# Kernel optimization log

Hardware: AMD Instinct MI355X
Metric: run time of the kernel (lower is better)

The kernel has to match this reference:

```python
import jax, jax.numpy as jnp
import numpy as np


def _grid_sample_3d(vol, grid):
    """Trilinear 3D grid_sample, zero padding, align_corners=False (torch default).

    vol:  [B, C, D, H, W]
    grid: [B, P, 3] normalized coords in [-1, 1]; grid[...,0]->W axis,
          grid[...,1]->H axis, grid[...,2]->D axis (torch convention).
    returns [B, C, P]
    """
    B, C, D, H, W = vol.shape
    x = (grid[..., 0] + 1.0) * (W * 0.5) - 0.5
    y = (grid[..., 1] + 1.0) * (H * 0.5) - 0.5
    z = (grid[..., 2] + 1.0) * (D * 0.5) - 0.5
    x0, y0, z0 = jnp.floor(x), jnp.floor(y), jnp.floor(z)
    gather = jax.vmap(lambda v, zz, yy, xx: v[:, zz, yy, xx])  # per-batch gather -> [C, P]
    out = jnp.zeros((B, C, x.shape[1]), vol.dtype)
    for dz in (0.0, 1.0):
        for dy in (0.0, 1.0):
            for dx in (0.0, 1.0):
                xi, yi, zi = x0 + dx, y0 + dy, z0 + dz
                w = (1.0 - jnp.abs(x - xi)) * (1.0 - jnp.abs(y - yi)) * (1.0 - jnp.abs(z - zi))
                valid = (xi >= 0) & (xi < W) & (yi >= 0) & (yi < H) & (zi >= 0) & (zi < D)
                xc = jnp.clip(xi, 0, W - 1).astype(jnp.int32)
                yc = jnp.clip(yi, 0, H - 1).astype(jnp.int32)
                zc = jnp.clip(zi, 0, D - 1).astype(jnp.int32)
                vals = gather(vol, zc, yc, xc)  # [B, C, P]
                out = out + vals * jnp.where(valid, w, 0.0)[:, None, :]
    return out


def _offset_grid(xs, A, Wk):
    """xs: [N,3] sample points; A: [N,3,3]; Wk: [3,K] offset weights.
    Returns [N, K, 3] grid coords ordered (z_feat, y_feat, x_feat) as in the torch code."""
    off = jnp.einsum('nij,jk->nik', A, Wk)  # bmm with repeated weight -> [N,3,K]
    xf = xs[:, 2:3] + off[:, 0, :]
    yf = xs[:, 1:2] + off[:, 1, :]
    zf = xs[:, 0:1] + off[:, 2, :]
    return jnp.stack([zf, yf, xf], axis=-1)


def setup_inputs() -> dict:
    key = jax.random.key(0)
    k1, k2, k3, k4 = jax.random.split(key, 4)
    B, C, D, H, W = 2, 16, 96, 96, 96
    Feats, K = 512, 1024
    inp = jax.random.normal(k1, (B, C, D, H, W), jnp.float32)
    xyz_sample = jax.random.uniform(k2, (B, Feats, 3), jnp.float32, -1.0, 1.0)
    A = jax.random.normal(k3, (B * Feats, 3, 3), jnp.float32) * 0.1
    weight = jax.random.normal(k4, (6, K), jnp.float32) * 0.05  # xyz_off.weight
    return {"input": inp, "xyz_sample": xyz_sample, "A": A, "weight": weight}


def reference(input, xyz_sample, A, weight):
    B, Feats, _ = xyz_sample.shape
    C = input.shape[1]
    K = weight.shape[1]  # 1024
    xs = xyz_sample.reshape(B * Feats, 3)
    g1 = _offset_grid(xs, A, weight[:3]).reshape(B, Feats * K, 3)
    g2 = _offset_grid(xs, A, weight[3:]).reshape(B, Feats * K, 3)
    feats = _grid_sample_3d(input, g1) - _grid_sample_3d(input, g2)  # [B, C, Feats*K]
    return feats.reshape(B, C * Feats, K)
```

## Files before the change

### kernel.cpp

```cpp
#include <hip/hip_runtime.h>


#define NB 2
#define NC 16
#define NS 96
#define NS3 (NS * NS * NS)
#define FEATS 512
#define NK 1024
#define KSPLIT 2
#define KCHUNK (NK / KSPLIT)
#define PASSES 4

#define RVOX 8
#define VSTRIDE 48

__device__ __forceinline__ unsigned int bfround(float f) {
  unsigned int u = __float_as_uint(f);
  return (u + 0x7fffu + ((u >> 16) & 1u)) >> 16;
}

#define BLO(v) __uint_as_float((v) << 16)
#define BHI(v) __uint_as_float((v) & 0xffff0000u)

__device__ __forceinline__ void tri_duo(
    const float* __restrict__ vol, size_t cbase,
    const unsigned char* __restrict__ sp,
    int ox0, int oy0, int oz0,
    float x, float y, float z, float sgn, float acc[8]) {
  float fx0 = floorf(x), fy0 = floorf(y), fz0 = floorf(z);
  int ix0 = (int)fx0, iy0 = (int)fy0, iz0 = (int)fz0;
  float tx = x - fx0, ty = y - fy0, tz = z - fz0;
  float wxa[2] = {1.0f - tx, tx};
  float wya[2] = {1.0f - ty, ty};
  float wza[2] = {1.0f - tz, tz};

  int lx0 = ix0 - ox0, ly0 = iy0 - oy0, lz0 = iz0 - oz0;
  bool fast = ((unsigned)lx0 < 7u) & ((unsigned)ly0 < 7u) & ((unsigned)lz0 < 7u);

  if (__builtin_expect(fast, 1)) {
#pragma unroll
    for (int dz = 0; dz < 2; dz++) {
      float wz = sgn * wza[dz];
#pragma unroll
      for (int dy = 0; dy < 2; dy++) {
        float wzy = wz * wya[dy];
        const unsigned char* rp =
            sp + (((lz0 + dz) * RVOX + (ly0 + dy)) * RVOX + lx0) * VSTRIDE;
#pragma unroll
        for (int dx = 0; dx < 2; dx++) {
          float w = wzy * wxa[dx];
          uint4 u = *(const uint4*)(rp + dx * VSTRIDE);
          acc[0] += w * BLO(u.x);
          acc[1] += w * BHI(u.x);
          acc[2] += w * BLO(u.y);
          acc[3] += w * BHI(u.y);
          acc[4] += w * BLO(u.z);
          acc[5] += w * BHI(u.z);
          acc[6] += w * BLO(u.w);
          acc[7] += w * BHI(u.w);
        }
      }
    }
  } else {
#pragma unroll
    for (int dz = 0; dz < 2; dz++) {
      int zc = iz0 + dz;
      if ((unsigned)zc >= (unsigned)NS) continue;
#pragma unroll
      for (int dy = 0; dy < 2; dy++) {
        int yc = iy0 + dy;
        if ((unsigned)yc >= (unsigned)NS) continue;
        float wzy = sgn * wza[dz] * wya[dy];
#pragma unroll
        for (int dx = 0; dx < 2; dx++) {
          int xc = ix0 + dx;
          if ((unsigned)xc >= (unsigned)NS) continue;
          float w = wzy * wxa[dx];
          const float* p = vol + cbase + (((size_t)zc * NS + yc) * NS + xc);
#pragma unroll
          for (int c = 0; c < 8; c++)
            acc[c] += w * p[(size_t)c * NS3];
        }
      }
    }
  }
}

__global__ __launch_bounds__(256) void sample_fused(
    const float* __restrict__ vol, const float* __restrict__ xyz,
    const float* __restrict__ A, const float* __restrict__ weight,
    float* __restrict__ out) {
  __shared__ __align__(16) unsigned char stage[RVOX * RVOX * RVOX * VSTRIDE];

  int bid = blockIdx.x;
  int kseg = bid & (KSPLIT - 1);
  int n = bid >> 1;
  int b = n >> 9;
  int f = n & 511;
  int kbase = kseg * KCHUNK;
  int tid = threadIdx.x;

  const float* Xn = xyz + (size_t)n * 3;
  float bx = (Xn[0] + 1.0f) * 48.0f - 0.5f;
  float by = (Xn[1] + 1.0f) * 48.0f - 0.5f;
  float bz = (Xn[2] + 1.0f) * 48.0f - 0.5f;
  int ox0 = (int)floorf(bx) - 3;
  int oy0 = (int)floorf(by) - 3;
  int oz0 = (int)floorf(bz) - 3;

  int duo = tid & 1;
  int ksub = tid >> 1;

  float wreg[PASSES][6];
#pragma unroll
  for (int p = 0; p < PASSES; p++) {
    int k = kbase + p * 128 + ksub;
#pragma unroll
    for (int q = 0; q < 6; q++) wreg[p][q] = weight[q * NK + k];
  }

  const float* An = A + (size_t)n * 9;
  float a00 = An[0], a01 = An[1], a02 = An[2];
  float a10 = An[3], a11 = An[4], a12 = An[5];
  float a20 = An[6], a21 = An[7], a22 = An[8];

  size_t vb = (size_t)b * NC * NS3;
#pragma unroll
  for (int j = 0; j < 4; j++) {
    int w = tid + 256 * j;
    int half = w & 1;
    int v = w >> 1;
    int xg = v & 7, yg = (v >> 3) & 7, zg = v >> 6;
    int xc = ox0 + xg, yc = oy0 + yg, zc = oz0 + zg;
    uint4 r = make_uint4(0u, 0u, 0u, 0u);
    if (((unsigned)xc < (unsigned)NS) & ((unsigned)yc < (unsigned)NS) &
        ((unsigned)zc < (unsigned)NS)) {
      const float* p = vol + vb + (size_t)(half * 8) * NS3 +
                       (((size_t)zc * NS + yc) * NS + xc);
      float f0 = p[0];
      float f1 = p[NS3];
      float f2 = p[2 * NS3];
      float f3 = p[3 * NS3];
      float f4 = p[4 * NS3];
      float f5 = p[5 * NS3];
      float f6 = p[6 * NS3];
      float f7 = p[7 * NS3];
      r.x = bfround(f0) | (bfround(f1) << 16);
      r.y = bfround(f2) | (bfround(f3) << 16);
      r.z = bfround(f4) | (bfround(f5) << 16);
      r.w = bfround(f6) | (bfround(f7) << 16);
    }
    *(uint4*)(stage + (size_t)v * VSTRIDE + half * 16) = r;
  }
  __syncthreads();

  const unsigned char* sp = stage + duo * 16;
  size_t cbase = ((size_t)b * NC + duo * 8) * NS3;
  size_t obase = (size_t)b * (NC * FEATS * NK) +
                 (size_t)(duo * 8) * (FEATS * NK) + (size_t)f * NK + kbase;

#pragma unroll
  for (int pass = 0; pass < PASSES; pass++) {
    int kl = pass * 128 + ksub;
    float w0 = wreg[pass][0];
    float w1 = wreg[pass][1];
    float w2 = wreg[pass][2];
    float w3 = wreg[pass][3];
    float w4 = wreg[pass][4];
    float w5 = wreg[pass][5];

    float acc[8] = {0.0f, 0.0f, 0.0f, 0.0f, 0.0f, 0.0f, 0.0f, 0.0f};

    {
      float oz = a00 * w0 + a01 * w1 + a02 * w2;
      float oy = a10 * w0 + a11 * w1 + a12 * w2;
      float ox = a20 * w0 + a21 * w1 + a22 * w2;
      tri_duo(vol, cbase, sp, ox0, oy0, oz0, bx + ox * 48.0f, by + oy * 48.0f,
              bz + oz * 48.0f, 1.0f, acc);
    }
    {
      float oz = a00 * w3 + a01 * w4 + a02 * w5;
      float oy = a10 * w3 + a11 * w4 + a12 * w5;
      float ox = a20 * w3 + a21 * w4 + a22 * w5;
      tri_duo(vol, cbase, sp, ox0, oy0, oz0, bx + ox * 48.0f, by + oy * 48.0f,
              bz + oz * 48.0f, -1.0f, acc);
    }

    size_t o = obase + kl;
#pragma unroll
    for (int c = 0; c < 8; c++)
      out[o + (size_t)c * (FEATS * NK)] = acc[c];
  }
}

extern "C" void kernel_launch(void* const* d_in, const int* in_sizes, int n_in,
                              void* d_out, int out_size, void* d_ws,
                              size_t ws_size, hipStream_t stream) {
  const float* vol    = (const float*)d_in[0];
  const float* xyz    = (const float*)d_in[1];
  const float* A      = (const float*)d_in[2];
  const float* weight = (const float*)d_in[3];
  float* out = (float*)d_out;

  sample_fused<<<NB * FEATS * KSPLIT, 256, 0, stream>>>(vol, xyz, A, weight,
                                                        out);
}
```

Baseline: 200.0 us.

## Drop K-split, swizzle LDS staging layout, and software-pipeline weight loads

Each block now handles all 1024 offsets for one feature point, so the 8x8x8 neighbourhood is staged into shared memory once instead of twice. The stage moves to a 64-byte stride with an XOR swizzle on the y/x and z/half bits to cut LDS bank conflicts on the uint4 reads. Weight loads are prefetched one pass ahead in a rolled loop instead of all preloaded into registers. The trade-off is half as many blocks (less parallelism and tail balance), larger shared memory per block, and more address arithmetic per sample.

```diff
diff --git a/kernel.cpp b/kernel.cpp
--- a/kernel.cpp
+++ b/kernel.cpp
@@ -7,12 +7,16 @@
 #define NS3 (NS * NS * NS)
 #define FEATS 512
 #define NK 1024
-#define KSPLIT 2
-#define KCHUNK (NK / KSPLIT)
-#define PASSES 4
+#define PASSES 8
 
 #define RVOX 8
-#define VSTRIDE 48
+
+__device__ __forceinline__ int stage_addr(int xg, int yg, int zg, int h) {
+  int v = (zg << 6) + (yg << 3) + xg;
+  int sw1 = (yg ^ (xg >> 1)) & 1;
+  int sw2 = (h ^ zg) & 1;
+  return (v << 6) | (sw1 << 5) | (sw2 << 4);
+}
 
 __device__ __forceinline__ unsigned int bfround(float f) {
   unsigned int u = __float_as_uint(f);
@@ -24,7 +28,7 @@
 
 __device__ __forceinline__ void tri_duo(
     const float* __restrict__ vol, size_t cbase,
-    const unsigned char* __restrict__ sp,
+    const unsigned char* __restrict__ stage, int duo,
     int ox0, int oy0, int oz0,
     float x, float y, float z, float sgn, float acc[8]) {
   float fx0 = floorf(x), fy0 = floorf(y), fz0 = floorf(z);
@@ -41,15 +45,16 @@
 #pragma unroll
     for (int dz = 0; dz < 2; dz++) {
       float wz = sgn * wza[dz];
+      int vz = lz0 + dz;
 #pragma unroll
       for (int dy = 0; dy < 2; dy++) {
         float wzy = wz * wya[dy];
-        const unsigned char* rp =
-            sp + (((lz0 + dz) * RVOX + (ly0 + dy)) * RVOX + lx0) * VSTRIDE;
+        int vy = ly0 + dy;
 #pragma unroll
         for (int dx = 0; dx < 2; dx++) {
           float w = wzy * wxa[dx];
-          uint4 u = *(const uint4*)(rp + dx * VSTRIDE);
+          int vx = lx0 + dx;
+          uint4 u = *(const uint4*)(stage + stage_addr(vx, vy, vz, duo));
           acc[0] += w * BLO(u.x);
           acc[1] += w * BHI(u.x);
           acc[2] += w * BLO(u.y);
@@ -90,14 +95,11 @@
     const float* __restrict__ vol, const float* __restrict__ xyz,
     const float* __restrict__ A, const float* __restrict__ weight,
     float* __restrict__ out) {
-  __shared__ __align__(16) unsigned char stage[RVOX * RVOX * RVOX * VSTRIDE];
-
-  int bid = blockIdx.x;
-  int kseg = bid & (KSPLIT - 1);
-  int n = bid >> 1;
+  __shared__ __align__(128) unsigned char stage[RVOX * RVOX * RVOX * 64];
+
+  int n = blockIdx.x;
   int b = n >> 9;
   int f = n & 511;
-  int kbase = kseg * KCHUNK;
   int tid = threadIdx.x;
 
   const float* Xn = xyz + (size_t)n * 3;
@@ -110,14 +112,6 @@
 
   int duo = tid & 1;
   int ksub = tid >> 1;
-
-  float wreg[PASSES][6];
-#pragma unroll
-  for (int p = 0; p < PASSES; p++) {
-    int k = kbase + p * 128 + ksub;
-#pragma unroll
-    for (int q = 0; q < 6; q++) wreg[p][q] = weight[q * NK + k];
-  }
 
   const float* An = A + (size_t)n * 9;
   float a00 = An[0], a01 = An[1], a02 = An[2];
@@ -150,46 +144,49 @@
       r.z = bfround(f4) | (bfround(f5) << 16);
       r.w = bfround(f6) | (bfround(f7) << 16);
     }
-    *(uint4*)(stage + (size_t)v * VSTRIDE + half * 16) = r;
+    *(uint4*)(stage + stage_addr(xg, yg, zg, half)) = r;
   }
   __syncthreads();
 
-  const unsigned char* sp = stage + duo * 16;
   size_t cbase = ((size_t)b * NC + duo * 8) * NS3;
   size_t obase = (size_t)b * (NC * FEATS * NK) +
-                 (size_t)(duo * 8) * (FEATS * NK) + (size_t)f * NK + kbase;
-
-#pragma unroll
+                 (size_t)(duo * 8) * (FEATS * NK) + (size_t)f * NK;
+
+  float wc[6], wn[6];
+#pragma unroll
+  for (int q = 0; q < 6; q++) wc[q] = weight[q * NK + ksub];
+
   for (int pass = 0; pass < PASSES; pass++) {
     int kl = pass * 128 + ksub;
-    float w0 = wreg[pass][0];
-    float w1 = wreg[pass][1];
-    float w2 = wreg[pass][2];
-    float w3 = wreg[pass][3];
-    float w4 = wreg[pass][4];
-    float w5 = wreg[pass][5];
+    if (pass < PASSES - 1) {
+#pragma unroll
+      for (int q = 0; q < 6; q++) wn[q] = weight[q * NK + kl + 128];
+    }
 
     float acc[8] = {0.0f, 0.0f, 0.0f, 0.0f, 0.0f, 0.0f, 0.0f, 0.0f};
 
     {
-      float oz = a00 * w0 + a01 * w1 + a02 * w2;
-      float oy = a10 * w0 + a11 * w1 + a12 * w2;
-      float ox = a20 * w0 + a21 * w1 + a22 * w2;
-      tri_duo(vol, cbase, sp, ox0, oy0, oz0, bx + ox * 48.0f, by + oy * 48.0f,
-              bz + oz * 48.0f, 1.0f, acc);
+      float oz = a00 * wc[0] + a01 * wc[1] + a02 * wc[2];
+      float oy = a10 * wc[0] + a11 * wc[1] + a12 * wc[2];
+      float ox = a20 * wc[0] + a21 * wc[1] + a22 * wc[2];
+      tri_duo(vol, cbase, stage, duo, ox0, oy0, oz0, bx + ox * 48.0f,
+              by + oy * 48.0f, bz + oz * 48.0f, 1.0f, acc);
     }
     {
-      float oz = a00 * w3 + a01 * w4 + a02 * w5;
-      float oy = a10 * w3 + a11 * w4 + a12 * w5;
-      float ox = a20 * w3 + a21 * w4 + a22 * w5;
-      tri_duo(vol, cbase, sp, ox0, oy0, oz0, bx + ox * 48.0f, by + oy * 48.0f,
-              bz + oz * 48.0f, -1.0f, acc);
+      float oz = a00 * wc[3] + a01 * wc[4] + a02 * wc[5];
+      float oy = a10 * wc[3] + a11 * wc[4] + a12 * wc[5];
+      float ox = a20 * wc[3] + a21 * wc[4] + a22 * wc[5];
+      tri_duo(vol, cbase, stage, duo, ox0, oy0, oz0, bx + ox * 48.0f,
+              by + oy * 48.0f, bz + oz * 48.0f, -1.0f, acc);
     }
 
     size_t o = obase + kl;
 #pragma unroll
     for (int c = 0; c < 8; c++)
       out[o + (size_t)c * (FEATS * NK)] = acc[c];
+
+#pragma unroll
+    for (int q = 0; q < 6; q++) wc[q] = wn[q];
   }
 }
 
@@ -202,6 +199,5 @@
   const float* weight = (const float*)d_in[3];
   float* out = (float*)d_out;
 
-  sample_fused<<<NB * FEATS * KSPLIT, 256, 0, stream>>>(vol, xyz, A, weight,
-                                                        out);
-}
+  sample_fused<<<NB * FEATS, 256, 0, stream>>>(vol, xyz, A, weight, out);
+}
```

Result: slower. 204.0 us (+2.0%).
